# Optimization experiments

Hardware: AMD Instinct MI355X
Metric: run time of the kernel (lower is better)

## Reference

```python
import jax, jax.numpy as jnp
import numpy as np


def conv2d(x, w, b, stride, pad):
    y = jax.lax.conv_general_dilated(
        x, w, (stride, stride), [(pad, pad), (pad, pad)],
        dimension_numbers=('NCHW', 'OIHW', 'NCHW'))
    return y + b[None, :, None, None]


def setup_inputs() -> dict:
    key = jax.random.key(0)
    ks = jax.random.split(key, 12)
    B = 8
    s = 0.02
    return {
        'x1': jax.random.normal(ks[0], (B, 256, 128, 128), jnp.float32),
        'x2': jax.random.normal(ks[1], (B, 512, 64, 64), jnp.float32),
        'x3': jax.random.normal(ks[2], (B, 1024, 32, 32), jnp.float32),
        'x4': jax.random.normal(ks[3], (B, 2048, 16, 16), jnp.float32),
        'cov1_w': jax.random.normal(ks[4], (512, 256, 3, 3), jnp.float32) * s,
        'cov1_b': jnp.zeros((512,), jnp.float32),
        'cov2_w': jax.random.normal(ks[5], (512, 512, 3, 3), jnp.float32) * s,
        'cov2_b': jnp.zeros((512,), jnp.float32),
        'cov3_w': jax.random.normal(ks[6], (512, 1024, 3, 3), jnp.float32) * s,
        'cov3_b': jnp.zeros((512,), jnp.float32),
        'cov4_w': jax.random.normal(ks[7], (512, 2048, 1, 1), jnp.float32) * s,
        'cov4_b': jnp.zeros((512,), jnp.float32),
        'gce_fc1_w': jax.random.normal(ks[8], (8, 64, 256), jnp.float32) * s,
        'gce_fc1_b': jnp.zeros((8, 64), jnp.float32),
        'gce_fc2_w': jax.random.normal(ks[9], (8, 256, 64), jnp.float32) * s,
        'gce_fc2_b': jnp.zeros((8, 256), jnp.float32),
        'gce_sa_w': jax.random.normal(ks[10], (8, 256), jnp.float32) * s,
        'gce_sa_b': jnp.zeros((8,), jnp.float32),
    }


def reference(x1, x2, x3, x4,
              cov1_w, cov1_b, cov2_w, cov2_b, cov3_w, cov3_b, cov4_w, cov4_b,
              gce_fc1_w, gce_fc1_b, gce_fc2_w, gce_fc2_b, gce_sa_w, gce_sa_b):
    # NOTE (faithful to original): DSCA.forward overwrites its attention output
    # with `rearrange(x, 'b (h w) c -> b c h w')`, i.e. it returns its first
    # argument (cov4(x4)) unchanged. Hence cov1/cov2/cov3 and the whole
    # dynamic-top-k attention path are dead code with exactly-zero gradients;
    # omitting them yields identical outputs and identical (zero) grads.
    x4 = conv2d(x4, cov4_w, cov4_b, 1, 0)          # [B,512,16,16]
    x = jnp.concatenate([x4, x4, x4, x4], axis=1)  # [B,2048,16,16]
    x0 = x
    B, C, H, W = x.shape
    G = 8
    xg = x.reshape(B, G, C // G, H, W)             # [B,G,256,H,W]
    # ChannelAttention per group (reduction_ratio=4: 256->64->256)
    avg = xg.mean(axis=(3, 4))                                           # [B,G,256]
    h = jax.nn.relu(jnp.einsum('bgc,goc->bgo', avg, gce_fc1_w) + gce_fc1_b)
    ca = jax.nn.sigmoid(jnp.einsum('bgo,gco->bgc', h, gce_fc2_w) + gce_fc2_b)
    y = xg * ca[:, :, :, None, None]
    # SpatialAttention per group (1x1 conv to 1 channel)
    sa = jax.nn.sigmoid(jnp.einsum('bgchw,gc->bghw', y, gce_sa_w)
                        + gce_sa_b[None, :, None, None])
    y = y * sa[:, :, None, :, :]
    # GroupCBAMEnhancer gating: sigmoid, then hard-1 above per-group mean
    y = jax.nn.sigmoid(y)
    mean = y.mean(axis=(2, 3, 4), keepdims=True)   # mean over (c,h,w) per group
    mask = jnp.where(y > mean, jnp.float32(1.0), y).reshape(B, C, H, W)
    return x * mask + x0
```

## Files before the change

### kernel.cpp

```cpp
#include <hip/hip_runtime.h>
#include <math.h>

typedef __attribute__((ext_vector_type(8))) short bf16x8;
typedef __attribute__((ext_vector_type(8))) unsigned short u16x8;
typedef __attribute__((ext_vector_type(4))) float f32x4;

#define GLOAD_LDS16(g, l) __builtin_amdgcn_global_load_lds( \
    (const __attribute__((address_space(1))) unsigned int*)(g), \
    (__attribute__((address_space(3))) unsigned int*)(l), 16, 0, 0)

__device__ __forceinline__ unsigned short f2bf(float f) {
    unsigned int u = __builtin_bit_cast(unsigned int, f);
    unsigned int r = (u + 0x7FFFu + ((u >> 16) & 1)) >> 16;
    return (unsigned short)r;
}

__device__ __forceinline__ float sigmoidf_(float v) {
    return 1.f / (1.f + expf(-v));
}

__global__ __launch_bounds__(256) void convert_kernel(
    const float* __restrict__ w, const float* __restrict__ x4,
    unsigned short* __restrict__ wbf, unsigned short* __restrict__ xbf)
{
    __shared__ float t[64][65];
    if (blockIdx.x < 512) {
        int f = blockIdx.x * 256 + threadIdx.x;
        int tile = f >> 9, inner = f & 511;
        int r = inner >> 3, cc = inner & 7;
        int mt = tile >> 5, kt = tile & 31;
        const float* src = w + (mt * 64 + r) * 2048 + kt * 64 + cc * 8;
        float4 v0 = *(const float4*)src;
        float4 v1 = *(const float4*)(src + 4);
        u16x8 o;
        o[0] = f2bf(v0.x); o[1] = f2bf(v0.y); o[2] = f2bf(v0.z); o[3] = f2bf(v0.w);
        o[4] = f2bf(v1.x); o[5] = f2bf(v1.y); o[6] = f2bf(v1.z); o[7] = f2bf(v1.w);
        *(u16x8*)(wbf + (size_t)tile * 4096 + r * 64 + ((cc ^ (r & 7)) * 8)) = o;
        return;
    }
    const int bi = blockIdx.x - 512;
    const int b = bi >> 7, rem = bi & 127;
    const int kt = rem >> 2, pg = rem & 3;
    const float* src = x4 + ((size_t)b * 2048 + kt * 64) * 256 + pg * 64;
#pragma unroll
    for (int i = 0; i < 4; ++i) {
        int f = i * 256 + threadIdx.x;
        int kk = f >> 4, pp4 = f & 15;
        float4 v = *(const float4*)(src + kk * 256 + pp4 * 4);
        t[pp4 * 4 + 0][kk] = v.x;
        t[pp4 * 4 + 1][kk] = v.y;
        t[pp4 * 4 + 2][kk] = v.z;
        t[pp4 * 4 + 3][kk] = v.w;
    }
    __syncthreads();
    unsigned short* dst = xbf + (size_t)((b * 4 + pg) * 32 + kt) * 4096;
#pragma unroll
    for (int i = 0; i < 2; ++i) {
        int inner = i * 256 + threadIdx.x;
        int r = inner >> 3, cc = inner & 7;
        u16x8 o;
#pragma unroll
        for (int j = 0; j < 8; ++j) o[j] = f2bf(t[r][cc * 8 + j]);
        *(u16x8*)(dst + r * 64 + ((cc ^ (r & 7)) * 8)) = o;
    }
}

__global__ __launch_bounds__(256) void gemm_bf16(
    const unsigned short* __restrict__ wbf, const unsigned short* __restrict__ xbf,
    float* __restrict__ partial)
{
    __shared__ short As[2][4096];
    __shared__ short Bs[2][4096];

    const int tid = threadIdx.x;
    const int wave = tid >> 6, lane = tid & 63;
    const int wm = wave >> 1, wn = wave & 1;
    const int lr = lane & 15, lh = lane >> 4;

    const int nt = blockIdx.x, mt = blockIdx.y, ks = blockIdx.z;

    const unsigned short* Abase = wbf + (size_t)(mt * 32 + ks * 16) * 4096;
    const unsigned short* Bbase = xbf + (size_t)(nt * 32 + ks * 16) * 4096;

#define STAGE(buf, t)                                                         \
    {                                                                         \
        const unsigned short* A_ = Abase + (t) * 4096;                        \
        const unsigned short* B_ = Bbase + (t) * 4096;                        \
        _Pragma("unroll")                                                     \
        for (int q = 0; q < 2; ++q) {                                         \
            int seg = (q * 4 + wave) * 512;                                   \
            GLOAD_LDS16(A_ + seg + lane * 8, &As[buf][seg]);                  \
            GLOAD_LDS16(B_ + seg + lane * 8, &Bs[buf][seg]);                  \
        }                                                                     \
    }

    STAGE(0, 0);
    __syncthreads();

    f32x4 acc[2][2] = {};
    int cur = 0;
    for (int t = 0; t < 16; ++t) {
        if (t < 15) STAGE(cur ^ 1, t + 1);
#pragma unroll
        for (int kc = 0; kc < 2; ++kc) {
            const int ch = kc * 4 + lh;
            int rA0 = wm * 32 + lr, rA1 = rA0 + 16;
            int rB0 = wn * 32 + lr, rB1 = rB0 + 16;
            bf16x8 a0 = *(const bf16x8*)(&As[cur][rA0 * 64 + (ch ^ (rA0 & 7)) * 8]);
            bf16x8 a1 = *(const bf16x8*)(&As[cur][rA1 * 64 + (ch ^ (rA1 & 7)) * 8]);
            bf16x8 b0 = *(const bf16x8*)(&Bs[cur][rB0 * 64 + (ch ^ (rB0 & 7)) * 8]);
            bf16x8 b1 = *(const bf16x8*)(&Bs[cur][rB1 * 64 + (ch ^ (rB1 & 7)) * 8]);
            acc[0][0] = __builtin_amdgcn_mfma_f32_16x16x32_bf16(a0, b0, acc[0][0], 0, 0, 0);
            acc[0][1] = __builtin_amdgcn_mfma_f32_16x16x32_bf16(a0, b1, acc[0][1], 0, 0, 0);
            acc[1][0] = __builtin_amdgcn_mfma_f32_16x16x32_bf16(a1, b0, acc[1][0], 0, 0, 0);
            acc[1][1] = __builtin_amdgcn_mfma_f32_16x16x32_bf16(a1, b1, acc[1][1], 0, 0, 0);
        }
        __syncthreads();
        cur ^= 1;
    }
#undef STAGE

    float* pb = partial + ((size_t)ks * 512 + mt * 64) * 2048 + nt * 64;
#pragma unroll
    for (int i = 0; i < 2; ++i)
#pragma unroll
        for (int j = 0; j < 2; ++j)
#pragma unroll
            for (int rr = 0; rr < 4; ++rr) {
                int m = wm * 32 + i * 16 + lh * 4 + rr;
                int n = wn * 32 + j * 16 + lr;
                pb[m * 2048 + n] = acc[i][j][rr];
            }
}

__global__ __launch_bounds__(256) void reduce_bias(
    const float* __restrict__ partial, const float* __restrict__ bias,
    float* __restrict__ y4, float* __restrict__ chansum)
{
    int f = blockIdx.x * 256 + threadIdx.x;
    int m = f >> 9, n4 = f & 511;
    float4 a = ((const float4*)partial)[f];
    float4 c = ((const float4*)partial)[f + 262144];
    float bv = bias[m];
    float4 o;
    o.x = a.x + c.x + bv; o.y = a.y + c.y + bv;
    o.z = a.z + c.z + bv; o.w = a.w + c.w + bv;
    int b = n4 >> 6, p4 = n4 & 63;
    *(float4*)(y4 + ((size_t)(b * 512 + m)) * 256 + p4 * 4) = o;
    float s = o.x + o.y + o.z + o.w;
#pragma unroll
    for (int off = 32; off > 0; off >>= 1) s += __shfl_down(s, off);
    if ((threadIdx.x & 63) == 0) chansum[b * 512 + m] = s * (1.f / 256.f);
}

__global__ __launch_bounds__(256) void sa_kernel(
    const float* __restrict__ y4, const float* __restrict__ chansum,
    const float* __restrict__ fc1w, const float* __restrict__ fc1b,
    const float* __restrict__ fc2w, const float* __restrict__ fc2b,
    const float* __restrict__ saw, const float* __restrict__ sab,
    float* __restrict__ ca, float* __restrict__ sa, float* __restrict__ gsums)
{
    const int blk = blockIdx.x;
    const int bg = blk >> 3, pc = blk & 7;
    const int b = bg >> 3, g = bg & 7;
    const int tid = threadIdx.x;
    const float* xg = y4 + ((size_t)b * 512 + (g & 1) * 256) * 256;

    __shared__ float avgs[256], red[256], hs[64], cas[256], caws[256], sas[32];

    avgs[tid] = chansum[b * 512 + (g & 1) * 256 + tid];
    __syncthreads();
    {
        int o = tid & 63, seg = tid >> 6;
        const float* wr = fc1w + (g * 64 + o) * 256 + seg * 64;
        const float* av = avgs + seg * 64;
        float s = 0.f;
#pragma unroll
        for (int i = 0; i < 64; ++i) s = fmaf(av[i], wr[i], s);
        red[tid] = s;
    }
    __syncthreads();
    if (tid < 64) {
        float s = fc1b[g * 64 + tid] + red[tid] + red[64 + tid] + red[128 + tid] + red[192 + tid];
        hs[tid] = fmaxf(s, 0.f);
    }
    __syncthreads();
    {
        const float* wr = fc2w + (g * 256 + tid) * 64;
        float s = fc2b[g * 256 + tid];
#pragma unroll
        for (int i = 0; i < 64; ++i) s = fmaf(hs[i], wr[i], s);
        float v = sigmoidf_(s);
        cas[tid] = v;
        caws[tid] = v * saw[g * 256 + tid];
        if (pc == 0) ca[bg * 256 + tid] = v;
    }
    __syncthreads();
    const int p_l = tid & 31, seg8 = tid >> 5;
    const int p = pc * 32 + p_l;
    {
        float s = 0.f;
#pragma unroll
        for (int i = 0; i < 32; ++i) {
            int c = seg8 * 32 + i;
            s = fmaf(xg[c * 256 + p], caws[c], s);
        }
        red[tid] = s;
    }
    __syncthreads();
    if (tid < 32) {
        float s = sab[g];
#pragma unroll
        for (int k = 0; k < 8; ++k) s += red[k * 32 + tid];
        float v = sigmoidf_(s);
        sas[tid] = v;
        sa[bg * 256 + pc * 32 + tid] = v;
    }
    __syncthreads();
    {
        float sv = sas[p_l];
        float s = 0.f;
#pragma unroll
        for (int i = 0; i < 32; ++i) {
            int c = seg8 * 32 + i;
            s += sigmoidf_(xg[c * 256 + p] * cas[c] * sv);
        }
        red[tid] = s;
    }
    __syncthreads();
    for (int off = 128; off > 0; off >>= 1) {
        if (tid < off) red[tid] += red[tid + off];
        __syncthreads();
    }
    if (tid == 0) gsums[blk] = red[0];
}

__global__ __launch_bounds__(256) void final_kernel(
    const float* __restrict__ y4, const float* __restrict__ ca,
    const float* __restrict__ sa, const float* __restrict__ gsums,
    float* __restrict__ out)
{
    int f = blockIdx.x * 256 + threadIdx.x;
    int p4 = f & 63, ch = (f >> 6) & 2047, b = f >> 17;
    int g = ch >> 8, c = ch & 255, bg = b * 8 + g;
    const float4 x = *(const float4*)(y4 + ((size_t)b * 512 + (g & 1) * 256 + c) * 256 + p4 * 4);
    float cav = ca[bg * 256 + c];
    const float4 sv = *(const float4*)(sa + bg * 256 + p4 * 4);
    float msum = 0.f;
#pragma unroll
    for (int i = 0; i < 8; ++i) msum += gsums[bg * 8 + i];
    float mean = msum * (1.f / 65536.f);
    float4 o;
#define DOLANE(X) { float yv = sigmoidf_(x.X * cav * sv.X); float mk = (yv > mean) ? 1.f : yv; o.X = x.X * (1.f + mk); }
    DOLANE(x) DOLANE(y) DOLANE(z) DOLANE(w)
#undef DOLANE
    *(float4*)(out + (size_t)f * 4) = o;
}

extern "C" void kernel_launch(void* const* d_in, const int* in_sizes, int n_in,
                              void* d_out, int out_size, void* d_ws, size_t ws_size,
                              hipStream_t stream) {
    const float* x4   = (const float*)d_in[3];
    const float* w4   = (const float*)d_in[10];
    const float* b4   = (const float*)d_in[11];
    const float* fc1w = (const float*)d_in[12];
    const float* fc1b = (const float*)d_in[13];
    const float* fc2w = (const float*)d_in[14];
    const float* fc2b = (const float*)d_in[15];
    const float* saw  = (const float*)d_in[16];
    const float* sab  = (const float*)d_in[17];
    float* out = (float*)d_out;

    float* ws = (float*)d_ws;
    float* y4      = ws;
    float* ca      = ws + 1048576;
    float* sa      = ws + 1064960;
    float* gsums   = ws + 1081344;
    float* chansum = ws + 1081856;
    float* partial = ws + 1085952;
    unsigned short* wbf = (unsigned short*)(ws + 3183104);
    unsigned short* xbf = (unsigned short*)(ws + 3707392);

    convert_kernel<<<dim3(1536), dim3(256), 0, stream>>>(w4, x4, wbf, xbf);
    gemm_bf16<<<dim3(32, 8, 2), dim3(256), 0, stream>>>(wbf, xbf, partial);
    reduce_bias<<<dim3(1024), dim3(256), 0, stream>>>(partial, b4, y4, chansum);
    sa_kernel<<<dim3(512), dim3(256), 0, stream>>>(y4, chansum, fc1w, fc1b, fc2w, fc2b,
                                                   saw, sab, ca, sa, gsums);
    final_kernel<<<dim3(4096), dim3(256), 0, stream>>>(y4, ca, sa, gsums, out);
}
```

Before: 50.88 us.

## Replace split-K GEMM with M-split tiles and fuse bias/channel-sum epilogue

```diff
diff --git a/kernel.cpp b/kernel.cpp
--- a/kernel.cpp
+++ b/kernel.cpp
@@ -67,9 +67,10 @@
 
 __global__ __launch_bounds__(256) void gemm_bf16(
     const unsigned short* __restrict__ wbf, const unsigned short* __restrict__ xbf,
-    float* __restrict__ partial)
-{
-    __shared__ short As[2][4096];
+    const float* __restrict__ bias, float* __restrict__ y4,
+    float* __restrict__ chanpart)
+{
+    __shared__ short As[2][2048];
     __shared__ short Bs[2][4096];
 
     const int tid = threadIdx.x;
@@ -77,84 +78,71 @@
     const int wm = wave >> 1, wn = wave & 1;
     const int lr = lane & 15, lh = lane >> 4;
 
-    const int nt = blockIdx.x, mt = blockIdx.y, ks = blockIdx.z;
-
-    const unsigned short* Abase = wbf + (size_t)(mt * 32 + ks * 16) * 4096;
-    const unsigned short* Bbase = xbf + (size_t)(nt * 32 + ks * 16) * 4096;
+    const int nt = blockIdx.x;
+    const int mt = blockIdx.y;
+
+    const unsigned short* Abase = wbf + ((size_t)(mt >> 1) * 32) * 4096 + (mt & 1) * 2048;
+    const unsigned short* Bbase = xbf + (size_t)nt * 32 * 4096;
 
 #define STAGE(buf, t)                                                         \
     {                                                                         \
-        const unsigned short* A_ = Abase + (t) * 4096;                        \
-        const unsigned short* B_ = Bbase + (t) * 4096;                        \
+        const unsigned short* A_ = Abase + (size_t)(t) * 4096;                \
+        const unsigned short* B_ = Bbase + (size_t)(t) * 4096;                \
         _Pragma("unroll")                                                     \
-        for (int q = 0; q < 2; ++q) {                                         \
-            int seg = (q * 4 + wave) * 512;                                   \
-            GLOAD_LDS16(A_ + seg + lane * 8, &As[buf][seg]);                  \
-            GLOAD_LDS16(B_ + seg + lane * 8, &Bs[buf][seg]);                  \
+        for (int q2 = 0; q2 < 3; ++q2) {                                      \
+            int seg = wave * 3 + q2;                                          \
+            if (seg < 4) {                                                    \
+                GLOAD_LDS16(A_ + seg * 512 + lane * 8, &As[buf][seg * 512]);  \
+            } else {                                                          \
+                GLOAD_LDS16(B_ + (seg - 4) * 512 + lane * 8,                  \
+                            &Bs[buf][(seg - 4) * 512]);                       \
+            }                                                                 \
         }                                                                     \
     }
 
     STAGE(0, 0);
     __syncthreads();
 
-    f32x4 acc[2][2] = {};
+    f32x4 acc[2] = {};
     int cur = 0;
-    for (int t = 0; t < 16; ++t) {
-        if (t < 15) STAGE(cur ^ 1, t + 1);
+    for (int t = 0; t < 32; ++t) {
+        if (t < 31) STAGE(cur ^ 1, t + 1);
 #pragma unroll
         for (int kc = 0; kc < 2; ++kc) {
             const int ch = kc * 4 + lh;
-            int rA0 = wm * 32 + lr, rA1 = rA0 + 16;
+            int rA  = wm * 16 + lr;
             int rB0 = wn * 32 + lr, rB1 = rB0 + 16;
-            bf16x8 a0 = *(const bf16x8*)(&As[cur][rA0 * 64 + (ch ^ (rA0 & 7)) * 8]);
-            bf16x8 a1 = *(const bf16x8*)(&As[cur][rA1 * 64 + (ch ^ (rA1 & 7)) * 8]);
-            bf16x8 b0 = *(const bf16x8*)(&Bs[cur][rB0 * 64 + (ch ^ (rB0 & 7)) * 8]);
-            bf16x8 b1 = *(const bf16x8*)(&Bs[cur][rB1 * 64 + (ch ^ (rB1 & 7)) * 8]);
-            acc[0][0] = __builtin_amdgcn_mfma_f32_16x16x32_bf16(a0, b0, acc[0][0], 0, 0, 0);
-            acc[0][1] = __builtin_amdgcn_mfma_f32_16x16x32_bf16(a0, b1, acc[0][1], 0, 0, 0);
-            acc[1][0] = __builtin_amdgcn_mfma_f32_16x16x32_bf16(a1, b0, acc[1][0], 0, 0, 0);
-            acc[1][1] = __builtin_amdgcn_mfma_f32_16x16x32_bf16(a1, b1, acc[1][1], 0, 0, 0);
+            bf16x8 a0 = *(const bf16x8*)(&As[cur][rA  * 64 + ((ch ^ (rA  & 7)) * 8)]);
+            bf16x8 b0 = *(const bf16x8*)(&Bs[cur][rB0 * 64 + ((ch ^ (rB0 & 7)) * 8)]);
+            bf16x8 b1 = *(const bf16x8*)(&Bs[cur][rB1 * 64 + ((ch ^ (rB1 & 7)) * 8)]);
+            acc[0] = __builtin_amdgcn_mfma_f32_16x16x32_bf16(a0, b0, acc[0], 0, 0, 0);
+            acc[1] = __builtin_amdgcn_mfma_f32_16x16x32_bf16(a0, b1, acc[1], 0, 0, 0);
         }
         __syncthreads();
         cur ^= 1;
     }
 #undef STAGE
 
-    float* pb = partial + ((size_t)ks * 512 + mt * 64) * 2048 + nt * 64;
-#pragma unroll
-    for (int i = 0; i < 2; ++i)
-#pragma unroll
-        for (int j = 0; j < 2; ++j)
-#pragma unroll
-            for (int rr = 0; rr < 4; ++rr) {
-                int m = wm * 32 + i * 16 + lh * 4 + rr;
-                int n = wn * 32 + j * 16 + lr;
-                pb[m * 2048 + n] = acc[i][j][rr];
-            }
-}
-
-__global__ __launch_bounds__(256) void reduce_bias(
-    const float* __restrict__ partial, const float* __restrict__ bias,
-    float* __restrict__ y4, float* __restrict__ chansum)
-{
-    int f = blockIdx.x * 256 + threadIdx.x;
-    int m = f >> 9, n4 = f & 511;
-    float4 a = ((const float4*)partial)[f];
-    float4 c = ((const float4*)partial)[f + 262144];
-    float bv = bias[m];
-    float4 o;
-    o.x = a.x + c.x + bv; o.y = a.y + c.y + bv;
-    o.z = a.z + c.z + bv; o.w = a.w + c.w + bv;
-    int b = n4 >> 6, p4 = n4 & 63;
-    *(float4*)(y4 + ((size_t)(b * 512 + m)) * 256 + p4 * 4) = o;
-    float s = o.x + o.y + o.z + o.w;
-#pragma unroll
-    for (int off = 32; off > 0; off >>= 1) s += __shfl_down(s, off);
-    if ((threadIdx.x & 63) == 0) chansum[b * 512 + m] = s * (1.f / 256.f);
+    const int b = nt >> 2, q = nt & 3;
+    float* yb = y4 + ((size_t)b * 512 + mt * 32) * 256 + q * 64;
+#pragma unroll
+    for (int rr = 0; rr < 4; ++rr) {
+        const int m = wm * 16 + lh * 4 + rr;
+        const float bv = bias[mt * 32 + m];
+        yb[m * 256 + wn * 32 + lr]      = acc[0][rr] + bv;
+        yb[m * 256 + wn * 32 + 16 + lr] = acc[1][rr] + bv;
+        float s = acc[0][rr] + acc[1][rr];
+        s += __shfl_xor(s, 1);
+        s += __shfl_xor(s, 2);
+        s += __shfl_xor(s, 4);
+        s += __shfl_xor(s, 8);
+        if (lr == 0)
+            chanpart[(size_t)(b * 512 + mt * 32 + m) * 8 + q * 2 + wn] = s + 32.f * bv;
+    }
 }
 
 __global__ __launch_bounds__(256) void sa_kernel(
-    const float* __restrict__ y4, const float* __restrict__ chansum,
+    const float* __restrict__ y4, const float* __restrict__ chanpart,
     const float* __restrict__ fc1w, const float* __restrict__ fc1b,
     const float* __restrict__ fc2w, const float* __restrict__ fc2b,
     const float* __restrict__ saw, const float* __restrict__ sab,
@@ -168,7 +156,13 @@
 
     __shared__ float avgs[256], red[256], hs[64], cas[256], caws[256], sas[32];
 
-    avgs[tid] = chansum[b * 512 + (g & 1) * 256 + tid];
+    {
+        const float* cpp = chanpart + (size_t)(b * 512 + (g & 1) * 256 + tid) * 8;
+        float cp = 0.f;
+#pragma unroll
+        for (int i = 0; i < 8; ++i) cp += cpp[i];
+        avgs[tid] = cp * (1.f / 256.f);
+    }
     __syncthreads();
     {
         int o = tid & 63, seg = tid >> 6;
@@ -272,19 +266,17 @@
     float* out = (float*)d_out;
 
     float* ws = (float*)d_ws;
-    float* y4      = ws;
-    float* ca      = ws + 1048576;
-    float* sa      = ws + 1064960;
-    float* gsums   = ws + 1081344;
-    float* chansum = ws + 1081856;
-    float* partial = ws + 1085952;
-    unsigned short* wbf = (unsigned short*)(ws + 3183104);
-    unsigned short* xbf = (unsigned short*)(ws + 3707392);
+    float* y4       = ws;
+    float* ca       = ws + 1048576;
+    float* sa       = ws + 1064960;
+    float* gsums    = ws + 1081344;
+    float* chanpart = ws + 1081856;
+    unsigned short* wbf = (unsigned short*)(ws + 1114624);
+    unsigned short* xbf = (unsigned short*)(ws + 1638912);
 
     convert_kernel<<<dim3(1536), dim3(256), 0, stream>>>(w4, x4, wbf, xbf);
-    gemm_bf16<<<dim3(32, 8, 2), dim3(256), 0, stream>>>(wbf, xbf, partial);
-    reduce_bias<<<dim3(1024), dim3(256), 0, stream>>>(partial, b4, y4, chansum);
-    sa_kernel<<<dim3(512), dim3(256), 0, stream>>>(y4, chansum, fc1w, fc1b, fc2w, fc2b,
+    gemm_bf16<<<dim3(32, 16), dim3(256), 0, stream>>>(wbf, xbf, b4, y4, chanpart);
+    sa_kernel<<<dim3(512), dim3(256), 0, stream>>>(y4, chanpart, fc1w, fc1b, fc2w, fc2b,
                                                    saw, sab, ca, sa, gsums);
     final_kernel<<<dim3(4096), dim3(256), 0, stream>>>(y4, ca, sa, gsums, out);
 }
```

Result: slower. 52.49 us (+3.2%).
